# Kernel optimization log

Measured on AMD Instinct MI355X. Metric: run time of the kernel, lower is better.

## Reference

```python
import jax, jax.numpy as jnp
import numpy as np

# ---- static config (mirrors Net.__init__) ----
N_NODES, N_EDGES = 4000, 20000
N_PROTS, D = 919, 512            # node_emb: Embedding(919, 512); F_in = D (divide_input=False)
TOWERS, F_OUT = 4, D // 4        # F_out = out_channels // towers = 128
EDGE_D = 50
N_GRAPHS, N_CLASSES = 32, 10
N_LAYERS = 2
EPS_BN, EPS_STD = 1e-5, 1e-5

# deg histogram passed to PNAConv; only avg_deg['log'] matters for the scalers used
DEG_HIST = np.array([0., 800., 1200., 900., 600., 300., 150., 50.])
AVG_DEG_LOG = float((np.log(np.arange(DEG_HIST.size) + 1.0) * DEG_HIST).sum() / DEG_HIST.sum())


def setup_inputs() -> dict:
    key = jax.random.key(0)
    ks = jax.random.split(key, 16)
    g = lambda i, shape, s=0.05: (jax.random.normal(ks[i], shape, jnp.float32) * s)
    return dict(
        node_emb_w=g(0, (N_PROTS, D), 0.1),
        edge_emb_w=g(1, (2, EDGE_D), 0.1),
        pe_w=g(2, (2, D)), pe_b=jnp.zeros((D,), jnp.float32),
        edge_enc_w=g(3, (N_LAYERS, EDGE_D, D)), edge_enc_b=jnp.zeros((N_LAYERS, D), jnp.float32),
        pre_w=g(4, (N_LAYERS, TOWERS, 3 * D, D)), pre_b=jnp.zeros((N_LAYERS, TOWERS, D), jnp.float32),
        post_w=g(5, (N_LAYERS, TOWERS, 13 * D, F_OUT)), post_b=jnp.zeros((N_LAYERS, TOWERS, F_OUT), jnp.float32),
        lin_w=g(6, (N_LAYERS, D, D)), lin_b=jnp.zeros((N_LAYERS, D), jnp.float32),
        bn_gamma=jnp.ones((N_LAYERS, D), jnp.float32), bn_beta=jnp.zeros((N_LAYERS, D), jnp.float32),
        acts=jax.random.normal(ks[7], (N_NODES, 2), jnp.float32),
        fc1_w=g(8, (D, 2 * D)), fc1_b=jnp.zeros((2 * D,), jnp.float32),
        fc_out_w=g(9, (2 * D, N_CLASSES)), fc_out_b=jnp.zeros((N_CLASSES,), jnp.float32),
        prelu_a=jnp.float32(0.25),
        global_idx=jax.random.randint(ks[10], (N_NODES,), 0, N_PROTS),
        sign=jax.random.randint(ks[11], (N_EDGES,), 0, 2),
        edge_index=jax.random.randint(ks[12], (2, N_EDGES), 0, N_NODES),
        batch=jnp.sort(jax.random.randint(ks[13], (N_NODES,), 0, N_GRAPHS)),
    )


def _pna_layer(x, src, dst, e, pre_w, pre_b, post_w, post_b, lin_w, lin_b):
    # x: [N, D], e: [E, D] (edge_encoder output), pre_w: [T, 3D, D], post_w: [T, 13D, F_OUT]
    N, E = x.shape[0], src.shape[0]
    # pre-NN on cat([x_i, x_j, edge_attr]) expressed as split matmuls (pre_layers=1 -> single Linear)
    Wi, Wj, We = pre_w[:, :D], pre_w[:, D:2 * D], pre_w[:, 2 * D:]
    m = (jnp.einsum('ef,tfd->etd', x[dst], Wi)
         + jnp.einsum('ef,tfd->etd', x[src], Wj)
         + jnp.einsum('ef,tfd->etd', e, We) + pre_b)          # [E, T, D]
    # multi-aggregation at destination nodes: mean / min / max / std
    cnt = jax.ops.segment_sum(jnp.ones((E,), m.dtype), dst, N)  # in-degree
    has = (cnt > 0)[:, None, None]
    deg = jnp.maximum(cnt, 1.0)[:, None, None]                  # clamp(1) as in PyG
    s1 = jax.ops.segment_sum(m, dst, N)
    s2 = jax.ops.segment_sum(m * m, dst, N)
    mean = s1 / deg
    std = jnp.sqrt(jax.nn.relu(s2 / deg - mean * mean) + EPS_STD)
    mn = jnp.where(has, jax.ops.segment_min(m, dst, N), 0.0)
    mx = jnp.where(has, jax.ops.segment_max(m, dst, N), 0.0)
    agg = jnp.concatenate([mean, mn, mx, std], axis=-1)         # [N, T, 4D]
    # degree scalers: identity, amplification, attenuation
    amp = jnp.log(deg + 1.0) / AVG_DEG_LOG
    out = jnp.concatenate([agg, agg * amp, agg / amp], axis=-1)  # [N, T, 12D]
    # post-NN on cat([x, out]) as split matmuls (post_layers=1)
    Wx, Wo = post_w[:, :D], post_w[:, D:]
    o = (jnp.einsum('nf,tfd->ntd', x, Wx)
         + jnp.einsum('ntf,tfd->ntd', out, Wo) + post_b)        # [N, T, F_OUT]
    return o.reshape(N, TOWERS * F_OUT) @ lin_w + lin_b         # [N, D]


def reference(node_emb_w, edge_emb_w, pe_w, pe_b, edge_enc_w, edge_enc_b,
              pre_w, pre_b, post_w, post_b, lin_w, lin_b, bn_gamma, bn_beta,
              acts, fc1_w, fc1_b, fc_out_w, fc_out_b, prelu_a,
              global_idx, sign, edge_index, batch):
    src, dst = edge_index[0], edge_index[1]
    x = node_emb_w[global_idx] + (acts @ pe_w + pe_b)           # node_emb + PostEncoding
    ea = edge_emb_w[sign]                                       # [E, 50]
    for l in range(N_LAYERS):
        e = ea @ edge_enc_w[l] + edge_enc_b[l]                  # shared edge encoder
        h = _pna_layer(x, src, dst, e, pre_w[l], pre_b[l], post_w[l], post_b[l], lin_w[l], lin_b[l])
        mu = h.mean(axis=0)
        var = ((h - mu) ** 2).mean(axis=0)                      # training-mode BatchNorm (biased var)
        x = jax.nn.relu(bn_gamma[l] * (h - mu) * jax.lax.rsqrt(var + EPS_BN) + bn_beta[l])
    pooled = jax.ops.segment_sum(x, batch, N_GRAPHS)            # global_add_pool
    z = pooled @ fc1_w + fc1_b
    z = jnp.where(z > 0, z, prelu_a * z)                        # PReLU
    logits = z @ fc_out_w + fc_out_b
    return jax.nn.log_softmax(logits, axis=-1)
```

## Files before the change

kernel.cpp:

```cpp
#include <hip/hip_runtime.h>
#include <hip/hip_bf16.h>
#include <float.h>

#define NN 4000
#define NE 20000
#define DD 512
#define NT 4
#define FO 128
#define NG 32
#define NC 10
#define XGW 4096
#define AVGLOG 1.2548916493836102f
#define EPS_STD_ 1e-5f
#define EPS_BN_ 1e-5f

typedef __bf16 bf16x8 __attribute__((ext_vector_type(8)));
typedef float  f32x4  __attribute__((ext_vector_type(4)));

__device__ __forceinline__ void async_copy16(const void* g, void* l) {
    __builtin_amdgcn_global_load_lds((const __attribute__((address_space(1))) void*)g,
                                     (__attribute__((address_space(3))) void*)l, 16, 0, 0);
}

__global__ __launch_bounds__(256) void k_xg(const __bf16* __restrict__ XB, const __bf16* __restrict__ WCAT,
                                            const float* __restrict__ pb,
                                            __bf16* __restrict__ XG, float* __restrict__ OF,
                                            float* __restrict__ BN, float* __restrict__ PL, int zero_pl) {
    const int m0 = blockIdx.y * 128, n0 = blockIdx.x * 128;
    __shared__ __bf16 As[128 * 32];
    __shared__ __bf16 Bs[128 * 32];
    const int tid = threadIdx.x;
    const int wave = tid >> 6, lane = tid & 63;
    const int wm = (wave >> 1) * 64, wn = (wave & 1) * 64;
    const int fr = lane & 15, fq = lane >> 4;
    const int fk = fq * 8;
    const int srow = lane >> 2, skc = (lane & 3) * 8;

    f32x4 acc[4][4];
    const f32x4 zero = {0.f, 0.f, 0.f, 0.f};
#pragma unroll
    for (int i = 0; i < 4; ++i)
#pragma unroll
        for (int j = 0; j < 4; ++j) acc[i][j] = zero;

    for (int k0 = 0; k0 < 512; k0 += 32) {
#pragma unroll
        for (int q = 0; q < 2; ++q) {
            const int row = wave * 32 + q * 16 + srow;
            int ar = m0 + row; if (ar > NN - 1) ar = NN - 1;
            async_copy16(XB + (size_t)ar * 512 + k0 + skc, As + wave * 1024 + q * 512);
            async_copy16(WCAT + (size_t)(n0 + row) * 512 + k0 + skc, Bs + wave * 1024 + q * 512);
        }
        __syncthreads();
        bf16x8 af[4], bfr[4];
#pragma unroll
        for (int mi = 0; mi < 4; ++mi) af[mi]  = *(const bf16x8*)(As + (wm + mi * 16 + fr) * 32 + fk);
#pragma unroll
        for (int ni = 0; ni < 4; ++ni) bfr[ni] = *(const bf16x8*)(Bs + (wn + ni * 16 + fr) * 32 + fk);
#pragma unroll
        for (int mi = 0; mi < 4; ++mi)
#pragma unroll
            for (int ni = 0; ni < 4; ++ni)
                acc[mi][ni] = __builtin_amdgcn_mfma_f32_16x16x32_bf16(af[mi], bfr[ni], acc[mi][ni], 0, 0, 0);
        __syncthreads();
    }
    if (n0 < 4096) {
#pragma unroll
        for (int mi = 0; mi < 4; ++mi) {
#pragma unroll
            for (int ni = 0; ni < 4; ++ni) {
                const int col = n0 + wn + ni * 16 + fr;
                const int rb = m0 + wm + mi * 16 + fq * 4;
#pragma unroll
                for (int r = 0; r < 4; ++r) {
                    const int rowc = rb + r;
                    if (rowc < NN) XG[(size_t)rowc * XGW + col] = (__bf16)acc[mi][ni][r];
                }
            }
        }
    } else {
        const int ocb = n0 - 4096;
#pragma unroll
        for (int mi = 0; mi < 4; ++mi) {
#pragma unroll
            for (int ni = 0; ni < 4; ++ni) {
                const int oc = ocb + wn + ni * 16 + fr;
                const float bv = pb[oc];
                const int rb = m0 + wm + mi * 16 + fq * 4;
#pragma unroll
                for (int r = 0; r < 4; ++r) {
                    const int rowc = rb + r;
                    if (rowc < NN) OF[(size_t)rowc * 512 + oc] = acc[mi][ni][r] + bv;
                }
            }
        }
    }
    if (blockIdx.x == 32 && blockIdx.y == 0) {
        BN[tid] = 0.f; BN[256 + tid] = 0.f; BN[512 + tid] = 0.f; BN[768 + tid] = 0.f;
        if (zero_pl)
            for (int i = tid; i < NG * DD; i += 256) PL[i] = 0.f;
    }
}

__global__ __launch_bounds__(256) void k_gw(const __bf16* __restrict__ AB, const __bf16* __restrict__ WTT,
                                            const float* __restrict__ amp, const float* __restrict__ ramp,
                                            __bf16* __restrict__ GWPb) {
    const int t = blockIdx.z & 3, kh = blockIdx.z >> 2;
    const int xg = blockIdx.x;
    const int m0 = blockIdx.y * 128;
    const __bf16* A  = AB  + (size_t)t * 2048 + (size_t)kh * 1024;
    const __bf16* BT = WTT + (size_t)t * 384 * 2048 + (size_t)xg * 128 * 2048 + (size_t)kh * 1024;
    __shared__ __bf16 As[128 * 32];
    __shared__ __bf16 Bs[128 * 32];
    const int tid = threadIdx.x;
    const int wave = tid >> 6, lane = tid & 63;
    const int wm = (wave >> 1) * 64, wn = (wave & 1) * 64;
    const int fr = lane & 15, fq = lane >> 4;
    const int fk = fq * 8;
    const int srow = lane >> 2, skc = (lane & 3) * 8;

    f32x4 acc[4][4];
    const f32x4 zero = {0.f, 0.f, 0.f, 0.f};
#pragma unroll
    for (int i = 0; i < 4; ++i)
#pragma unroll
        for (int j = 0; j < 4; ++j) acc[i][j] = zero;

    for (int k0 = 0; k0 < 1024; k0 += 32) {
#pragma unroll
        for (int q = 0; q < 2; ++q) {
            const int row = wave * 32 + q * 16 + srow;
            int ar = m0 + row; if (ar > NN - 1) ar = NN - 1;
            async_copy16(A + (size_t)ar * 8192 + k0 + skc, As + wave * 1024 + q * 512);
            async_copy16(BT + (size_t)row * 2048 + k0 + skc, Bs + wave * 1024 + q * 512);
        }
        __syncthreads();
        bf16x8 af[4], bfr[4];
#pragma unroll
        for (int mi = 0; mi < 4; ++mi) af[mi]  = *(const bf16x8*)(As + (wm + mi * 16 + fr) * 32 + fk);
#pragma unroll
        for (int ni = 0; ni < 4; ++ni) bfr[ni] = *(const bf16x8*)(Bs + (wn + ni * 16 + fr) * 32 + fk);
#pragma unroll
        for (int mi = 0; mi < 4; ++mi)
#pragma unroll
            for (int ni = 0; ni < 4; ++ni)
                acc[mi][ni] = __builtin_amdgcn_mfma_f32_16x16x32_bf16(af[mi], bfr[ni], acc[mi][ni], 0, 0, 0);
        __syncthreads();
    }
    const int p = xg * 2 + kh;
    __bf16* P = GWPb + (size_t)p * NN * 512 + (size_t)t * 128;
#pragma unroll
    for (int mi = 0; mi < 4; ++mi) {
        const int rb = m0 + wm + mi * 16 + fq * 4;
#pragma unroll
        for (int r = 0; r < 4; ++r) {
            const int row = rb + r;
            if (row < NN) {
                const float w = (xg == 0) ? 1.0f : (xg == 1 ? amp[row] : ramp[row]);
#pragma unroll
                for (int ni = 0; ni < 4; ++ni)
                    P[(size_t)row * 512 + wn + ni * 16 + fr] = (__bf16)(acc[mi][ni][r] * w);
            }
        }
    }
}

__global__ void k_combine(const float* __restrict__ OF, const __bf16* __restrict__ GWPb,
                          __bf16* __restrict__ OB) {
    const size_t idx8 = ((size_t)blockIdx.x * 256 + threadIdx.x) * 8;
    float4 o0 = *(const float4*)(OF + idx8);
    float4 o1 = *(const float4*)(OF + idx8 + 4);
    float s[8] = {o0.x, o0.y, o0.z, o0.w, o1.x, o1.y, o1.z, o1.w};
#pragma unroll
    for (int p = 0; p < 6; ++p) {
        bf16x8 g = *(const bf16x8*)(GWPb + (size_t)p * NN * 512 + idx8);
#pragma unroll
        for (int i = 0; i < 8; ++i) s[i] += (float)g[i];
    }
    bf16x8 ov;
#pragma unroll
    for (int i = 0; i < 8; ++i) ov[i] = (__bf16)s[i];
    *(bf16x8*)(OB + idx8) = ov;
}

__global__ __launch_bounds__(256) void k_lin(const __bf16* __restrict__ OB, const __bf16* __restrict__ WLINT,
                                             const float* __restrict__ bl, float* __restrict__ H,
                                             float* __restrict__ BN) {
    const int n0c = blockIdx.x * 128, m0 = blockIdx.y * 64;
    __shared__ __bf16 As[64 * 32];
    __shared__ __bf16 Bs[128 * 32];
    __shared__ float bnS[128], bnQ[128];
    const int tid = threadIdx.x;
    if (tid < 128) { bnS[tid] = 0.f; bnQ[tid] = 0.f; }
    const int wave = tid >> 6, lane = tid & 63;
    const int wr = wave >> 1, wc = wave & 1;
    const int fr = lane & 15, fq = lane >> 4;
    f32x4 acc[2][4];
    const f32x4 zero = {0.f, 0.f, 0.f, 0.f};
#pragma unroll
    for (int i = 0; i < 2; ++i)
#pragma unroll
        for (int j = 0; j < 4; ++j) acc[i][j] = zero;

    const int ar = tid >> 2, akc = (tid & 3) * 8;
    int arow = m0 + ar; if (arow > NN - 1) arow = NN - 1;
    for (int k0 = 0; k0 < 512; k0 += 32) {
        async_copy16(OB + (size_t)arow * 512 + k0 + akc, As + tid * 8);
#pragma unroll
        for (int i = 0; i < 2; ++i) {
            const int cb = tid + 256 * i;
            const int br = cb >> 2, bkc = (cb & 3) * 8;
            async_copy16(WLINT + (size_t)(n0c + br) * 512 + k0 + bkc, Bs + cb * 8);
        }
        __syncthreads();
        bf16x8 a[2], b[4];
#pragma unroll
        for (int mi = 0; mi < 2; ++mi) a[mi] = *(const bf16x8*)(As + (wr * 32 + mi * 16 + fr) * 32 + fq * 8);
#pragma unroll
        for (int ni = 0; ni < 4; ++ni) b[ni] = *(const bf16x8*)(Bs + (wc * 64 + ni * 16 + fr) * 32 + fq * 8);
#pragma unroll
        for (int mi = 0; mi < 2; ++mi)
#pragma unroll
            for (int ni = 0; ni < 4; ++ni)
                acc[mi][ni] = __builtin_amdgcn_mfma_f32_16x16x32_bf16(a[mi], b[ni], acc[mi][ni], 0, 0, 0);
        __syncthreads();
    }
#pragma unroll
    for (int ni = 0; ni < 4; ++ni) {
        const int lc = wc * 64 + ni * 16 + fr;
        const int col = n0c + lc;
        const float bv = bl[col];
        float s = 0.f, q = 0.f;
#pragma unroll
        for (int mi = 0; mi < 2; ++mi) {
#pragma unroll
            for (int r = 0; r < 4; ++r) {
                const int rowc = m0 + wr * 32 + mi * 16 + fq * 4 + r;
                if (rowc < NN) {
                    const float v = acc[mi][ni][r] + bv;
                    H[(size_t)rowc * 512 + col] = v;
                    s += v; q += v * v;
                }
            }
        }
        atomicAdd(&bnS[lc], s); atomicAdd(&bnQ[lc], q);
    }
    __syncthreads();
    if (tid < 128) {
        atomicAdd(&BN[n0c + tid], bnS[tid]);
        atomicAdd(&BN[512 + n0c + tid], bnQ[tid]);
    }
}

__device__ __forceinline__ void tr32(const float* __restrict__ S, int sld,
                                     __bf16* __restrict__ D, int dld, int tx, int ty) {
    __shared__ float t[32][33];
    const int y0 = ty * 4;
#pragma unroll
    for (int i = 0; i < 4; ++i) t[y0 + i][tx] = S[(size_t)(y0 + i) * sld + tx];
    __syncthreads();
#pragma unroll
    for (int i = 0; i < 4; ++i) D[(size_t)(y0 + i) * dld + tx] = (__bf16)t[tx][y0 + i];
}

__global__ __launch_bounds__(256) void k_tr(const float* __restrict__ pre_w, const float* __restrict__ post_w,
                                            const float* __restrict__ lin_w,
                                            const float* __restrict__ eemb, const float* __restrict__ eew_b,
                                            const float* __restrict__ eeb_b, const float* __restrict__ pre_b,
                                            __bf16* __restrict__ WCAT, __bf16* __restrict__ WTT,
                                            __bf16* __restrict__ WLINT, float* __restrict__ EM) {
    int id = blockIdx.x;
    const int lay = (id >= 5696) ? 1 : 0;
    id -= lay * 5696;
    const float* pw   = pre_w  + (size_t)lay * NT * 3 * 512 * 512;
    const float* pow_ = post_w + (size_t)lay * NT * 6656 * 128;
    const float* lw   = lin_w  + (size_t)lay * 512 * 512;
    const float* eew  = eew_b  + (size_t)lay * 50 * 512;
    const float* eeb  = eeb_b  + (size_t)lay * 512;
    const float* pb   = pre_b  + (size_t)lay * NT * 512;
    __bf16* WCATl  = WCAT  + (size_t)lay * 4608 * 512;
    __bf16* WTTl   = WTT   + (size_t)lay * NT * 384 * 2048;
    __bf16* WLINTl = WLINT + (size_t)lay * 512 * 512;
    float*  EMl    = EM    + (size_t)lay * 4096;
    const int tx = threadIdx.x & 31, ty = threadIdx.x >> 5;
    if (id < 2048) {
        const int z = id >> 8, r = id & 255;
        const int t = z & 3, half = z >> 2;
        const int x = r & 15, y = r >> 4;
        const float* S = pw + ((size_t)(t * 1536 + half * 512 + y * 32)) * 512 + x * 32;
        __bf16* D = WCATl + ((size_t)(half * 2048 + t * 512 + x * 32)) * 512 + y * 32;
        tr32(S, 512, D, 512, tx, ty);
    } else if (id < 2304) {
        const int id3 = id - 2048;
        const int t = id3 >> 6, r = id3 & 63;
        const int x = r & 3, y = r >> 2;
        const float* S = pow_ + ((size_t)(t * 6656 + y * 32)) * 128 + x * 32;
        __bf16* D = WCATl + ((size_t)(4096 + t * 128 + x * 32)) * 512 + y * 32;
        tr32(S, 128, D, 512, tx, ty);
    } else if (id < 5376) {
        const int id4 = id - 2304;
        const int z = id4 >> 8, r = id4 & 255;
        const int t = z / 3, w = z % 3;
        const int x = r & 3, y = r >> 2;
        const float* S = pow_ + ((size_t)(t * 6656 + 512 + w * 2048 + y * 32)) * 128 + x * 32;
        __bf16* D = WTTl + (size_t)t * 384 * 2048 + ((size_t)(w * 128 + x * 32)) * 2048 + y * 32;
        tr32(S, 128, D, 2048, tx, ty);
    } else if (id < 5632) {
        const int r = id - 5376;
        const int x = r & 15, y = r >> 4;
        const float* S = lw + (size_t)y * 32 * 512 + x * 32;
        __bf16* D = WLINTl + (size_t)x * 32 * 512 + y * 32;
        tr32(S, 512, D, 512, tx, ty);
    } else {
        __shared__ float eks[512];
        __shared__ float part[4][64];
        const int tid = threadIdx.x;
        const int id5 = id - 5632;
        const int k = id5 >> 5;
        const int g0 = (id5 & 31) * 64;
#pragma unroll
        for (int h = 0; h < 2; ++h) {
            const int f = tid + h * 256;
            float s = eeb[f];
            for (int c = 0; c < 50; ++c) s += eemb[k * 50 + c] * eew[(size_t)c * 512 + f];
            eks[f] = s;
        }
        __syncthreads();
        const int wave = tid >> 6, lane = tid & 63;
        const int g = g0 + lane;
        const int t = g >> 9, d = g & 511;
        const float* Wp = pw + ((size_t)(t * 1536 + 1024)) * 512 + d;
        float s = 0.f;
        const int f0 = wave * 128;
#pragma unroll 4
        for (int f = f0; f < f0 + 128; ++f) s += eks[f] * Wp[(size_t)f * 512];
        part[wave][lane] = s;
        __syncthreads();
        if (tid < 64) {
            const int gg = g0 + tid;
            EMl[k * 2048 + gg] = pb[gg] + part[0][tid] + part[1][tid] + part[2][tid] + part[3][tid];
        }
    }
}

__global__ void k_count(const int* __restrict__ dst, int* __restrict__ cnt) {
    int e = blockIdx.x * 256 + threadIdx.x;
    if (e < NE) atomicAdd(&cnt[dst[e]], 1);
}

__global__ __launch_bounds__(1024) void k_scan_bx(const int* __restrict__ cnt, int* __restrict__ offs,
                                                  float* __restrict__ amp, float* __restrict__ ramp,
                                                  const float* __restrict__ nemb, const float* __restrict__ acts,
                                                  const float* __restrict__ pew, const float* __restrict__ peb,
                                                  const int* __restrict__ gidx, __bf16* __restrict__ XB) {
    const int t = threadIdx.x;
    if (blockIdx.x == 0) {
        __shared__ int part[1024];
        const int base = t * 4;
        int loc[4]; int s = 0;
#pragma unroll
        for (int i = 0; i < 4; ++i) { int v = (base + i < NN) ? cnt[base + i] : 0; loc[i] = s; s += v; }
        part[t] = s;
        __syncthreads();
        for (int o = 1; o < 1024; o <<= 1) {
            int v = (t >= o) ? part[t - o] : 0;
            __syncthreads();
            part[t] += v;
            __syncthreads();
        }
        const int pre = (t > 0) ? part[t - 1] : 0;
#pragma unroll
        for (int i = 0; i < 4; ++i) if (base + i < NN) offs[base + i] = pre + loc[i];
        if (t == 1023) offs[NN] = part[1023];
        for (int n = t; n < NN; n += 1024) {
            float deg = fmaxf((float)cnt[n], 1.0f);
            float a = logf(deg + 1.0f) / AVGLOG;
            amp[n] = a; ramp[n] = 1.0f / a;
        }
    } else {
        const int idx = (blockIdx.x - 1) * 1024 + t;
        const int n = idx >> 9, d = idx & 511;
        float v = nemb[(size_t)gidx[n] * DD + d] + acts[n * 2] * pew[d] + acts[n * 2 + 1] * pew[DD + d] + peb[d];
        XB[idx] = (__bf16)v;
    }
}

__global__ void k_fill(const int* __restrict__ src, const int* __restrict__ dst,
                       const int* __restrict__ sgn, const int* __restrict__ offs,
                       int* __restrict__ fill, int* __restrict__ esrc, int* __restrict__ esgn) {
    int e = blockIdx.x * 256 + threadIdx.x;
    if (e < NE) {
        int d = dst[e];
        int pos = offs[d] + atomicAdd(&fill[d], 1);
        esrc[pos] = src[e];
        esgn[pos] = sgn[e];
    }
}

__global__ __launch_bounds__(256) void k_agg(const __bf16* __restrict__ XG, const float* __restrict__ EM,
                                             const int* __restrict__ offs, const int* __restrict__ cnt,
                                             const int* __restrict__ esrc, const int* __restrict__ esgn,
                                             __bf16* __restrict__ AB) {
    const int n = blockIdx.x;
    const int g = threadIdx.x * 8;
    float xid[8], em0[8], em1[8];
    {
        bf16x8 xb = *(const bf16x8*)(XG + (size_t)n * XGW + g);
#pragma unroll
        for (int i = 0; i < 8; ++i) xid[i] = (float)xb[i];
    }
    *(float4*)&em0[0] = *(const float4*)&EM[g];
    *(float4*)&em0[4] = *(const float4*)&EM[g + 4];
    *(float4*)&em1[0] = *(const float4*)&EM[2048 + g];
    *(float4*)&em1[4] = *(const float4*)&EM[2048 + g + 4];
    float s1[8], s2[8], mn[8], mx[8];
#pragma unroll
    for (int i = 0; i < 8; ++i) { s1[i] = 0.f; s2[i] = 0.f; mn[i] = FLT_MAX; mx[i] = -FLT_MAX; }
    const int j0 = offs[n], j1 = offs[n + 1];
    for (int j = j0; j < j1; ++j) {
        const int s = esrc[j];
        const int sg = esgn[j];
        bf16x8 xv = *(const bf16x8*)(XG + (size_t)s * XGW + 2048 + g);
#pragma unroll
        for (int i = 0; i < 8; ++i) {
            float m = xid[i] + (float)xv[i] + (sg ? em1[i] : em0[i]);
            s1[i] += m; s2[i] += m * m;
            mn[i] = fminf(mn[i], m); mx[i] = fmaxf(mx[i], m);
        }
    }
    const int c = cnt[n];
    const float deg = fmaxf((float)c, 1.0f);
    const float rdeg = 1.0f / deg;
    bf16x8 vmean, vmn, vmx, vsd;
#pragma unroll
    for (int i = 0; i < 8; ++i) {
        float mean = s1[i] * rdeg;
        float var = s2[i] * rdeg - mean * mean;
        float sd = sqrtf(fmaxf(var, 0.f) + EPS_STD_);
        float mnv = (c == 0) ? 0.f : mn[i];
        float mxv = (c == 0) ? 0.f : mx[i];
        vmean[i] = (__bf16)mean; vmn[i] = (__bf16)mnv; vmx[i] = (__bf16)mxv; vsd[i] = (__bf16)sd;
    }
    const int t = g >> 9, d = g & 511;
    __bf16* base = AB + (size_t)n * 8192 + (size_t)t * 2048 + d;
    *(bf16x8*)(base + 0 * DD) = vmean;
    *(bf16x8*)(base + 1 * DD) = vmn;
    *(bf16x8*)(base + 2 * DD) = vmx;
    *(bf16x8*)(base + 3 * DD) = vsd;
}

__global__ void k_bnapply(const float* __restrict__ H, const float* __restrict__ BN,
                          const float* __restrict__ gamma, const float* __restrict__ beta,
                          __bf16* __restrict__ XB, float* __restrict__ PL,
                          const int* __restrict__ batch, int last) {
    int idx = blockIdx.x * 256 + threadIdx.x;
    int n = idx >> 9, d = idx & 511;
    float mu = BN[d] * (1.0f / NN);
    float var = BN[512 + d] * (1.0f / NN) - mu * mu;
    float v = gamma[d] * (H[idx] - mu) * rsqrtf(var + EPS_BN_) + beta[d];
    v = fmaxf(v, 0.f);
    if (last) atomicAdd(&PL[(size_t)batch[n] * DD + d], v);
    else XB[idx] = (__bf16)v;
}

__global__ __launch_bounds__(128) void k_fc1(const float* __restrict__ PL, const float* __restrict__ W1,
                                             const float* __restrict__ b1, const float* __restrict__ pa,
                                             float* __restrict__ Z) {
    const int g = blockIdx.x >> 3;
    const int j = (blockIdx.x & 7) * 128 + threadIdx.x;
    __shared__ float pl[512];
    for (int i = threadIdx.x; i < 512; i += 128) pl[i] = PL[(size_t)g * 512 + i];
    __syncthreads();
    const float* w = W1 + j;
    float s0 = 0.f, s1 = 0.f, s2 = 0.f, s3 = 0.f;
#pragma unroll 2
    for (int f = 0; f < 512; f += 4) {
        s0 += pl[f + 0] * w[(size_t)(f + 0) * 1024];
        s1 += pl[f + 1] * w[(size_t)(f + 1) * 1024];
        s2 += pl[f + 2] * w[(size_t)(f + 2) * 1024];
        s3 += pl[f + 3] * w[(size_t)(f + 3) * 1024];
    }
    float s = b1[j] + ((s0 + s1) + (s2 + s3));
    const float a = *pa;
    Z[(size_t)g * 1024 + j] = s > 0.f ? s : a * s;
}

__global__ __launch_bounds__(64) void k_out(const float* __restrict__ Z, const float* __restrict__ Wo,
                                            const float* __restrict__ bo, float* __restrict__ out) {
    const int g = blockIdx.x, t = threadIdx.x;
    float part[NC];
#pragma unroll
    for (int c = 0; c < NC; ++c) part[c] = 0.f;
    for (int f = t; f < 1024; f += 64) {
        const float zv = Z[(size_t)g * 1024 + f];
#pragma unroll
        for (int c = 0; c < NC; ++c) part[c] += zv * Wo[(size_t)f * NC + c];
    }
#pragma unroll
    for (int off = 32; off > 0; off >>= 1)
#pragma unroll
        for (int c = 0; c < NC; ++c) part[c] += __shfl_down(part[c], off);
    if (t == 0) {
        float lg[NC], mxv = -FLT_MAX;
#pragma unroll
        for (int c = 0; c < NC; ++c) { lg[c] = part[c] + bo[c]; mxv = fmaxf(mxv, lg[c]); }
        float se = 0.f;
#pragma unroll
        for (int c = 0; c < NC; ++c) se += expf(lg[c] - mxv);
        const float lse = mxv + logf(se);
#pragma unroll
        for (int c = 0; c < NC; ++c) out[g * NC + c] = lg[c] - lse;
    }
}

extern "C" void kernel_launch(void* const* d_in, const int* in_sizes, int n_in,
                              void* d_out, int out_size, void* d_ws, size_t ws_size,
                              hipStream_t stream) {
    const float* node_emb_w = (const float*)d_in[0];
    const float* edge_emb_w = (const float*)d_in[1];
    const float* pe_w   = (const float*)d_in[2];
    const float* pe_b   = (const float*)d_in[3];
    const float* edge_enc_w = (const float*)d_in[4];
    const float* edge_enc_b = (const float*)d_in[5];
    const float* pre_w  = (const float*)d_in[6];
    const float* pre_b  = (const float*)d_in[7];
    const float* post_w = (const float*)d_in[8];
    const float* post_b = (const float*)d_in[9];
    const float* lin_w  = (const float*)d_in[10];
    const float* lin_b  = (const float*)d_in[11];
    const float* bn_gamma = (const float*)d_in[12];
    const float* bn_beta  = (const float*)d_in[13];
    const float* acts   = (const float*)d_in[14];
    const float* fc1_w  = (const float*)d_in[15];
    const float* fc1_b  = (const float*)d_in[16];
    const float* fc_out_w = (const float*)d_in[17];
    const float* fc_out_b = (const float*)d_in[18];
    const float* prelu_a  = (const float*)d_in[19];
    const int* global_idx = (const int*)d_in[20];
    const int* sgn        = (const int*)d_in[21];
    const int* edge_index = (const int*)d_in[22];
    const int* batch      = (const int*)d_in[23];
    float* out = (float*)d_out;

    char* W = (char*)d_ws;
    size_t off = 0;
    auto alloc = [&](size_t bytes) { void* p = W + off; off += (bytes + 63) & ~(size_t)63; return p; };
    __bf16* XB    = (__bf16*)alloc((size_t)NN * DD * 2);
    float*  H     = (float*)alloc((size_t)NN * DD * 4);
    __bf16* XG    = (__bf16*)alloc((size_t)NN * XGW * 2);
    __bf16* AB    = (__bf16*)alloc((size_t)NN * 8192 * 2);
    float*  OF    = (float*)alloc((size_t)NN * DD * 4);
    __bf16* GWPb  = (__bf16*)alloc((size_t)6 * NN * 512 * 2);
    __bf16* OB    = (__bf16*)alloc((size_t)NN * DD * 2);
    __bf16* WCAT  = (__bf16*)alloc((size_t)2 * 4608 * 512 * 2);
    __bf16* WTT   = (__bf16*)alloc((size_t)2 * NT * 384 * 2048 * 2);
    __bf16* WLINT = (__bf16*)alloc((size_t)2 * 512 * 512 * 2);
    float*  EM    = (float*)alloc((size_t)2 * 2 * 2048 * 4);
    float*  BN    = (float*)alloc(1024 * 4);
    float*  PL    = (float*)alloc((size_t)NG * DD * 4);
    float*  ZB    = (float*)alloc((size_t)NG * 1024 * 4);
    float*  AMP   = (float*)alloc(NN * 4);
    float*  RAMP  = (float*)alloc(NN * 4);
    int*    CNT   = (int*)alloc(NN * 4);
    int*    FILL  = (int*)alloc(NN * 4);
    int*    OFFS  = (int*)alloc((NN + 1) * 4);
    int*    ESRC  = (int*)alloc(NE * 4);
    int*    ESGN  = (int*)alloc(NE * 4);

    const int* src = edge_index;
    const int* dst = edge_index + NE;

    hipMemsetAsync(CNT, 0, 2 * NN * sizeof(int), stream);
    k_count<<<(NE + 255) / 256, 256, 0, stream>>>(dst, CNT);
    k_scan_bx<<<2001, 1024, 0, stream>>>(CNT, OFFS, AMP, RAMP,
                                         node_emb_w, acts, pe_w, pe_b, global_idx, XB);
    k_fill<<<(NE + 255) / 256, 256, 0, stream>>>(src, dst, sgn, OFFS, FILL, ESRC, ESGN);
    k_tr<<<2 * 5696, 256, 0, stream>>>(pre_w, post_w, lin_w,
                                       edge_emb_w, edge_enc_w, edge_enc_b, pre_b,
                                       WCAT, WTT, WLINT, EM);

    for (int l = 0; l < 2; ++l) {
        const float* post_b_l = post_b + (size_t)l * NT * FO;
        const float* lin_b_l  = lin_b  + (size_t)l * DD;
        __bf16* WCATl  = WCAT  + (size_t)l * 4608 * 512;
        __bf16* WTTl   = WTT   + (size_t)l * NT * 384 * 2048;
        __bf16* WLINTl = WLINT + (size_t)l * 512 * 512;
        float*  EMl    = EM    + (size_t)l * 4096;

        k_xg<<<dim3(36, 32), 256, 0, stream>>>(XB, WCATl, post_b_l, XG, OF, BN, PL, l == 1);
        k_agg<<<NN, 256, 0, stream>>>(XG, EMl, OFFS, CNT, ESRC, ESGN, AB);
        k_gw<<<dim3(3, 32, 8), 256, 0, stream>>>(AB, WTTl, AMP, RAMP, GWPb);
        k_combine<<<NN * DD / 2048, 256, 0, stream>>>(OF, GWPb, OB);
        k_lin<<<dim3(4, 63), 256, 0, stream>>>(OB, WLINTl, lin_b_l, H, BN);
        k_bnapply<<<NN * DD / 256, 256, 0, stream>>>(H, BN, bn_gamma + (size_t)l * DD,
                                                     bn_beta + (size_t)l * DD, XB, PL, batch, l == 1);
    }

    k_fc1<<<256, 128, 0, stream>>>(PL, fc1_w, fc1_b, prelu_a, ZB);
    k_out<<<NG, 64, 0, stream>>>(ZB, fc_out_w, fc_out_b, out);
}
```

Before: 499.0 us.

## Double K-step in GEMM tiles and pack edge src/sign with LDS-staged aggregation

The k_xg and k_gw GEMMs now load two 32-wide K slices per barrier pair, which halves the number of __syncthreads and doubles the LDS footprint per block. The edge CSR arrays are packed into a single int holding src and sign. k_agg stages up to 64 packed edge entries in LDS and processes neighbours two at a time, so more gather loads are in flight. The larger LDS tiles may lower occupancy, and degree now comes from the offset array instead of the count array.

```diff
diff --git a/kernel.cpp b/kernel.cpp
--- a/kernel.cpp
+++ b/kernel.cpp
@@ -27,8 +27,8 @@
                                             __bf16* __restrict__ XG, float* __restrict__ OF,
                                             float* __restrict__ BN, float* __restrict__ PL, int zero_pl) {
     const int m0 = blockIdx.y * 128, n0 = blockIdx.x * 128;
-    __shared__ __bf16 As[128 * 32];
-    __shared__ __bf16 Bs[128 * 32];
+    __shared__ __bf16 As[2 * 128 * 32];
+    __shared__ __bf16 Bs[2 * 128 * 32];
     const int tid = threadIdx.x;
     const int wave = tid >> 6, lane = tid & 63;
     const int wm = (wave >> 1) * 64, wn = (wave & 1) * 64;
@@ -43,25 +43,33 @@
 #pragma unroll
         for (int j = 0; j < 4; ++j) acc[i][j] = zero;
 
-    for (int k0 = 0; k0 < 512; k0 += 32) {
-#pragma unroll
-        for (int q = 0; q < 2; ++q) {
-            const int row = wave * 32 + q * 16 + srow;
-            int ar = m0 + row; if (ar > NN - 1) ar = NN - 1;
-            async_copy16(XB + (size_t)ar * 512 + k0 + skc, As + wave * 1024 + q * 512);
-            async_copy16(WCAT + (size_t)(n0 + row) * 512 + k0 + skc, Bs + wave * 1024 + q * 512);
-        }
-        __syncthreads();
-        bf16x8 af[4], bfr[4];
-#pragma unroll
-        for (int mi = 0; mi < 4; ++mi) af[mi]  = *(const bf16x8*)(As + (wm + mi * 16 + fr) * 32 + fk);
-#pragma unroll
-        for (int ni = 0; ni < 4; ++ni) bfr[ni] = *(const bf16x8*)(Bs + (wn + ni * 16 + fr) * 32 + fk);
-#pragma unroll
-        for (int mi = 0; mi < 4; ++mi)
-#pragma unroll
-            for (int ni = 0; ni < 4; ++ni)
-                acc[mi][ni] = __builtin_amdgcn_mfma_f32_16x16x32_bf16(af[mi], bfr[ni], acc[mi][ni], 0, 0, 0);
+    for (int k0 = 0; k0 < 512; k0 += 64) {
+#pragma unroll
+        for (int p = 0; p < 2; ++p) {
+#pragma unroll
+            for (int q = 0; q < 2; ++q) {
+                const int row = wave * 32 + q * 16 + srow;
+                int ar = m0 + row; if (ar > NN - 1) ar = NN - 1;
+                async_copy16(XB + (size_t)ar * 512 + k0 + p * 32 + skc,
+                             As + p * 4096 + wave * 1024 + q * 512);
+                async_copy16(WCAT + (size_t)(n0 + row) * 512 + k0 + p * 32 + skc,
+                             Bs + p * 4096 + wave * 1024 + q * 512);
+            }
+        }
+        __syncthreads();
+#pragma unroll
+        for (int p = 0; p < 2; ++p) {
+            bf16x8 af[4], bfr[4];
+#pragma unroll
+            for (int mi = 0; mi < 4; ++mi) af[mi]  = *(const bf16x8*)(As + p * 4096 + (wm + mi * 16 + fr) * 32 + fk);
+#pragma unroll
+            for (int ni = 0; ni < 4; ++ni) bfr[ni] = *(const bf16x8*)(Bs + p * 4096 + (wn + ni * 16 + fr) * 32 + fk);
+#pragma unroll
+            for (int mi = 0; mi < 4; ++mi)
+#pragma unroll
+                for (int ni = 0; ni < 4; ++ni)
+                    acc[mi][ni] = __builtin_amdgcn_mfma_f32_16x16x32_bf16(af[mi], bfr[ni], acc[mi][ni], 0, 0, 0);
+        }
         __syncthreads();
     }
     if (n0 < 4096) {
@@ -110,8 +118,8 @@
     const int m0 = blockIdx.y * 128;
     const __bf16* A  = AB  + (size_t)t * 2048 + (size_t)kh * 1024;
     const __bf16* BT = WTT + (size_t)t * 384 * 2048 + (size_t)xg * 128 * 2048 + (size_t)kh * 1024;
-    __shared__ __bf16 As[128 * 32];
-    __shared__ __bf16 Bs[128 * 32];
+    __shared__ __bf16 As[2 * 128 * 32];
+    __shared__ __bf16 Bs[2 * 128 * 32];
     const int tid = threadIdx.x;
     const int wave = tid >> 6, lane = tid & 63;
     const int wm = (wave >> 1) * 64, wn = (wave & 1) * 64;
@@ -126,25 +134,33 @@
 #pragma unroll
         for (int j = 0; j < 4; ++j) acc[i][j] = zero;
 
-    for (int k0 = 0; k0 < 1024; k0 += 32) {
-#pragma unroll
-        for (int q = 0; q < 2; ++q) {
-            const int row = wave * 32 + q * 16 + srow;
-            int ar = m0 + row; if (ar > NN - 1) ar = NN - 1;
-            async_copy16(A + (size_t)ar * 8192 + k0 + skc, As + wave * 1024 + q * 512);
-            async_copy16(BT + (size_t)row * 2048 + k0 + skc, Bs + wave * 1024 + q * 512);
-        }
-        __syncthreads();
-        bf16x8 af[4], bfr[4];
-#pragma unroll
-        for (int mi = 0; mi < 4; ++mi) af[mi]  = *(const bf16x8*)(As + (wm + mi * 16 + fr) * 32 + fk);
-#pragma unroll
-        for (int ni = 0; ni < 4; ++ni) bfr[ni] = *(const bf16x8*)(Bs + (wn + ni * 16 + fr) * 32 + fk);
-#pragma unroll
-        for (int mi = 0; mi < 4; ++mi)
-#pragma unroll
-            for (int ni = 0; ni < 4; ++ni)
-                acc[mi][ni] = __builtin_amdgcn_mfma_f32_16x16x32_bf16(af[mi], bfr[ni], acc[mi][ni], 0, 0, 0);
+    for (int k0 = 0; k0 < 1024; k0 += 64) {
+#pragma unroll
+        for (int p = 0; p < 2; ++p) {
+#pragma unroll
+            for (int q = 0; q < 2; ++q) {
+                const int row = wave * 32 + q * 16 + srow;
+                int ar = m0 + row; if (ar > NN - 1) ar = NN - 1;
+                async_copy16(A + (size_t)ar * 8192 + k0 + p * 32 + skc,
+                             As + p * 4096 + wave * 1024 + q * 512);
+                async_copy16(BT + (size_t)row * 2048 + k0 + p * 32 + skc,
+                             Bs + p * 4096 + wave * 1024 + q * 512);
+            }
+        }
+        __syncthreads();
+#pragma unroll
+        for (int p = 0; p < 2; ++p) {
+            bf16x8 af[4], bfr[4];
+#pragma unroll
+            for (int mi = 0; mi < 4; ++mi) af[mi]  = *(const bf16x8*)(As + p * 4096 + (wm + mi * 16 + fr) * 32 + fk);
+#pragma unroll
+            for (int ni = 0; ni < 4; ++ni) bfr[ni] = *(const bf16x8*)(Bs + p * 4096 + (wn + ni * 16 + fr) * 32 + fk);
+#pragma unroll
+            for (int mi = 0; mi < 4; ++mi)
+#pragma unroll
+                for (int ni = 0; ni < 4; ++ni)
+                    acc[mi][ni] = __builtin_amdgcn_mfma_f32_16x16x32_bf16(af[mi], bfr[ni], acc[mi][ni], 0, 0, 0);
+        }
         __syncthreads();
     }
     const int p = xg * 2 + kh;
@@ -387,22 +403,26 @@
 
 __global__ void k_fill(const int* __restrict__ src, const int* __restrict__ dst,
                        const int* __restrict__ sgn, const int* __restrict__ offs,
-                       int* __restrict__ fill, int* __restrict__ esrc, int* __restrict__ esgn) {
+                       int* __restrict__ fill, int* __restrict__ epack) {
     int e = blockIdx.x * 256 + threadIdx.x;
     if (e < NE) {
         int d = dst[e];
         int pos = offs[d] + atomicAdd(&fill[d], 1);
-        esrc[pos] = src[e];
-        esgn[pos] = sgn[e];
+        epack[pos] = (src[e] << 1) | sgn[e];
     }
 }
 
 __global__ __launch_bounds__(256) void k_agg(const __bf16* __restrict__ XG, const float* __restrict__ EM,
                                              const int* __restrict__ offs, const int* __restrict__ cnt,
-                                             const int* __restrict__ esrc, const int* __restrict__ esgn,
-                                             __bf16* __restrict__ AB) {
+                                             const int* __restrict__ epack, __bf16* __restrict__ AB) {
     const int n = blockIdx.x;
     const int g = threadIdx.x * 8;
+    __shared__ int se[64];
+    const int j0 = offs[n];
+    const int deg = offs[n + 1] - j0;
+    const int degc = deg < 64 ? deg : 64;
+    if (threadIdx.x < degc) se[threadIdx.x] = epack[j0 + threadIdx.x];
+    __syncthreads();
     float xid[8], em0[8], em1[8];
     {
         bf16x8 xb = *(const bf16x8*)(XG + (size_t)n * XGW + g);
@@ -416,21 +436,51 @@
     float s1[8], s2[8], mn[8], mx[8];
 #pragma unroll
     for (int i = 0; i < 8; ++i) { s1[i] = 0.f; s2[i] = 0.f; mn[i] = FLT_MAX; mx[i] = -FLT_MAX; }
-    const int j0 = offs[n], j1 = offs[n + 1];
-    for (int j = j0; j < j1; ++j) {
-        const int s = esrc[j];
-        const int sg = esgn[j];
-        bf16x8 xv = *(const bf16x8*)(XG + (size_t)s * XGW + 2048 + g);
+
+    int jj = 0;
+    for (; jj + 2 <= degc; jj += 2) {
+        const int e0 = se[jj], e1 = se[jj + 1];
+        bf16x8 x0 = *(const bf16x8*)(XG + (size_t)(e0 >> 1) * XGW + 2048 + g);
+        bf16x8 x1 = *(const bf16x8*)(XG + (size_t)(e1 >> 1) * XGW + 2048 + g);
+        const int sg0 = e0 & 1, sg1 = e1 & 1;
 #pragma unroll
         for (int i = 0; i < 8; ++i) {
-            float m = xid[i] + (float)xv[i] + (sg ? em1[i] : em0[i]);
+            float m = xid[i] + (float)x0[i] + (sg0 ? em1[i] : em0[i]);
             s1[i] += m; s2[i] += m * m;
             mn[i] = fminf(mn[i], m); mx[i] = fmaxf(mx[i], m);
         }
-    }
-    const int c = cnt[n];
-    const float deg = fmaxf((float)c, 1.0f);
-    const float rdeg = 1.0f / deg;
+#pragma unroll
+        for (int i = 0; i < 8; ++i) {
+            float m = xid[i] + (float)x1[i] + (sg1 ? em1[i] : em0[i]);
+            s1[i] += m; s2[i] += m * m;
+            mn[i] = fminf(mn[i], m); mx[i] = fmaxf(mx[i], m);
+        }
+    }
+    if (jj < degc) {
+        const int e0 = se[jj];
+        bf16x8 x0 = *(const bf16x8*)(XG + (size_t)(e0 >> 1) * XGW + 2048 + g);
+        const int sg0 = e0 & 1;
+#pragma unroll
+        for (int i = 0; i < 8; ++i) {
+            float m = xid[i] + (float)x0[i] + (sg0 ? em1[i] : em0[i]);
+            s1[i] += m; s2[i] += m * m;
+            mn[i] = fminf(mn[i], m); mx[i] = fmaxf(mx[i], m);
+        }
+    }
+    for (int j = 64; j < deg; ++j) {
+        const int e0 = epack[j0 + j];
+        bf16x8 x0 = *(const bf16x8*)(XG + (size_t)(e0 >> 1) * XGW + 2048 + g);
+        const int sg0 = e0 & 1;
+#pragma unroll
+        for (int i = 0; i < 8; ++i) {
+            float m = xid[i] + (float)x0[i] + (sg0 ? em1[i] : em0[i]);
+            s1[i] += m; s2[i] += m * m;
+            mn[i] = fminf(mn[i], m); mx[i] = fmaxf(mx[i], m);
+        }
+    }
+    const int c = deg;
+    const float degf = fmaxf((float)c, 1.0f);
+    const float rdeg = 1.0f / degf;
     bf16x8 vmean, vmn, vmx, vsd;
 #pragma unroll
     for (int i = 0; i < 8; ++i) {
@@ -564,8 +614,7 @@
     int*    CNT   = (int*)alloc(NN * 4);
     int*    FILL  = (int*)alloc(NN * 4);
     int*    OFFS  = (int*)alloc((NN + 1) * 4);
-    int*    ESRC  = (int*)alloc(NE * 4);
-    int*    ESGN  = (int*)alloc(NE * 4);
+    int*    EPACK = (int*)alloc(NE * 4);
 
     const int* src = edge_index;
     const int* dst = edge_index + NE;
@@ -574,7 +623,7 @@
     k_count<<<(NE + 255) / 256, 256, 0, stream>>>(dst, CNT);
     k_scan_bx<<<2001, 1024, 0, stream>>>(CNT, OFFS, AMP, RAMP,
                                          node_emb_w, acts, pe_w, pe_b, global_idx, XB);
-    k_fill<<<(NE + 255) / 256, 256, 0, stream>>>(src, dst, sgn, OFFS, FILL, ESRC, ESGN);
+    k_fill<<<(NE + 255) / 256, 256, 0, stream>>>(src, dst, sgn, OFFS, FILL, EPACK);
     k_tr<<<2 * 5696, 256, 0, stream>>>(pre_w, post_w, lin_w,
                                        edge_emb_w, edge_enc_w, edge_enc_b, pre_b,
                                        WCAT, WTT, WLINT, EM);
@@ -588,7 +637,7 @@
         float*  EMl    = EM    + (size_t)l * 4096;
 
         k_xg<<<dim3(36, 32), 256, 0, stream>>>(XB, WCATl, post_b_l, XG, OF, BN, PL, l == 1);
-        k_agg<<<NN, 256, 0, stream>>>(XG, EMl, OFFS, CNT, ESRC, ESGN, AB);
+        k_agg<<<NN, 256, 0, stream>>>(XG, EMl, OFFS, CNT, EPACK, AB);
         k_gw<<<dim3(3, 32, 8), 256, 0, stream>>>(AB, WTTl, AMP, RAMP, GWPb);
         k_combine<<<NN * DD / 2048, 256, 0, stream>>>(OF, GWPb, OB);
         k_lin<<<dim3(4, 63), 256, 0, stream>>>(OB, WLINTl, lin_b_l, H, BN);
```

Result: no change. 492.1 us (-1.4%).
